# Kernel tuning notes

Measured on AMD Instinct MI355X. Metric: run time of the kernel, lower is better.

Reference implementation:

```python
import jax, jax.numpy as jnp
import numpy as np

NUM_HEADS = 16
ROT_DIM = 128  # == head_dim here
ROPE_BASE = 10000.0

def _deinterleave(t):
    # non-HF RoPE layout fix: cat(even channels, odd channels) along head_dim
    return jnp.concatenate([t[..., ::2], t[..., 1::2]], axis=-1)

def _rope(t, cos, sin):
    # t: [B,S,H,D]; rotary applied to first ROT_DIM dims with half-split (GPT-NeoX style)
    rot, rest = t[..., :ROT_DIM], t[..., ROT_DIM:]
    x1, x2 = rot[..., : ROT_DIM // 2], rot[..., ROT_DIM // 2 :]
    c = cos[None, :, None, :]
    s = sin[None, :, None, :]
    rot = jnp.concatenate([x1 * c - x2 * s, x1 * s + x2 * c], axis=-1)
    return jnp.concatenate([rot, rest], axis=-1) if rest.shape[-1] else rot

def setup_inputs() -> dict:
    key = jax.random.key(0)
    ks = jax.random.split(key, 5)
    B, S, E = 4, 2048, 2048
    return {
        "x": jax.random.normal(ks[0], (B, S, E), jnp.float32),
        "wqkv_w": jax.random.normal(ks[1], (3 * E, E), jnp.float32) * (E ** -0.5),
        "wqkv_b": jax.random.normal(ks[2], (3 * E,), jnp.float32) * 0.01,
        "wo_w": jax.random.normal(ks[3], (E, E), jnp.float32) * (E ** -0.5),
        "wo_b": jax.random.normal(ks[4], (E,), jnp.float32) * 0.01,
    }

def reference(x, wqkv_w, wqkv_b, wo_w, wo_b):
    B, S, E = x.shape
    H = NUM_HEADS
    D = E // H
    scale = 1.0 / jnp.sqrt(jnp.asarray(D, x.dtype))
    # fused QKV projection; channel layout is (h, three, d)
    qkv = x @ wqkv_w.T + wqkv_b               # [B,S,3E]
    qkv = qkv.reshape(B, S, H, 3, D)
    q, k, v = qkv[..., 0, :], qkv[..., 1, :], qkv[..., 2, :]  # [B,S,H,D]
    # non-HF rotary layout shuffle on q,k only
    q = _deinterleave(q)
    k = _deinterleave(k)
    # rotary embedding
    inv_freq = 1.0 / (ROPE_BASE ** (jnp.arange(0, ROT_DIM, 2, dtype=jnp.float32) / ROT_DIM))
    t = jnp.arange(S, dtype=jnp.float32)
    freqs = jnp.outer(t, inv_freq)            # [S, ROT_DIM/2]
    cos, sin = jnp.cos(freqs).astype(x.dtype), jnp.sin(freqs).astype(x.dtype)
    q = _rope(q, cos, sin)
    k = _rope(k, cos, sin)
    # causal self-attention (vanilla, fp32 softmax)
    scores = jnp.einsum("bshd,bthd->bhst", q, k) * scale   # [B,H,S,S]
    causal = jnp.tril(jnp.ones((S, S), bool))
    scores = jnp.where(causal[None, None], scores, jnp.asarray(-1e4, scores.dtype))
    attn = jax.nn.softmax(scores.astype(jnp.float32), axis=-1).astype(scores.dtype)
    ctx = jnp.einsum("bhst,bthd->bshd", attn, v)           # [B,S,H,D]
    # output projection
    out = ctx.reshape(B, S, E) @ wo_w.T + wo_b
    return out
```

## Files before the change

kernel.cpp:

```cpp
#include <hip/hip_runtime.h>


using frag_ab = __attribute__((ext_vector_type(8))) short;
using frag_cd = __attribute__((ext_vector_type(4))) float;

__device__ __forceinline__ float b2f(unsigned short u) {
  union { unsigned int i; float f; } v; v.i = ((unsigned int)u) << 16; return v.f;
}
__device__ __forceinline__ unsigned short f2b(float f) {
  union { float f; unsigned int i; } v; v.f = f;
  unsigned int r = v.i + 0x7FFFu + ((v.i >> 16) & 1u);
  return (unsigned short)(r >> 16);
}
__device__ __forceinline__ unsigned int pack2(float a, float b) {
  return (unsigned int)f2b(a) | ((unsigned int)f2b(b) << 16);
}
__device__ __forceinline__ void gload16(const unsigned short* g, unsigned short* l) {
  __builtin_amdgcn_global_load_lds(
      (const __attribute__((address_space(1))) unsigned int*)g,
      (__attribute__((address_space(3))) unsigned int*)l, 16, 0, 0);
}

__global__ __launch_bounds__(256)
void cvt_f32_bf16(const float* __restrict__ in, unsigned short* __restrict__ out) {
  long i = (long)(blockIdx.x * 256 + threadIdx.x) * 8;
  float4 a = *(const float4*)&in[i];
  float4 b = *(const float4*)&in[i + 4];
  uint4 p;
  p.x = pack2(a.x, a.y); p.y = pack2(a.z, a.w);
  p.z = pack2(b.x, b.y); p.w = pack2(b.z, b.w);
  *(uint4*)&out[i] = p;
}

__device__ __forceinline__ void stage_a_async(const unsigned short* A, unsigned short* As,
                                              int row0, int k0, int wave, int lane, int ldk) {
#pragma unroll
  for (int i = 0; i < 4; i++) {
    int rbase = wave * 32 + i * 8;
    int r = rbase + (lane >> 3);
    int srcc = (lane & 7) ^ (r & 7);
    gload16(&A[(long)(row0 + r) * ldk + k0 + srcc * 8], &As[rbase * 64]);
  }
}
__device__ __forceinline__ void stage_b_cvt(const float* Bw, unsigned short* Bs,
                                            int row0, int k0, int tid) {
#pragma unroll
  for (int i = 0; i < 4; i++) {
    int c = tid + i * 256;
    int r = c >> 3, ch = c & 7;
    const float* src = &Bw[(long)(row0 + r) * 2048 + k0 + ch * 8];
    float4 v0 = *(const float4*)src;
    float4 v1 = *(const float4*)(src + 4);
    uint4 p;
    p.x = pack2(v0.x, v0.y); p.y = pack2(v0.z, v0.w);
    p.z = pack2(v1.x, v1.y); p.w = pack2(v1.z, v1.w);
    *(uint4*)&Bs[r * 64 + ((ch ^ (r & 7)) * 8)] = p;
  }
}

__global__ __launch_bounds__(256)
void gemm_qkv(const unsigned short* __restrict__ A,
              const float* __restrict__ Bw,
              const unsigned short* __restrict__ Bbf,
              const float* __restrict__ bias,
              unsigned short* __restrict__ Qb,
              unsigned short* __restrict__ Kb,
              unsigned short* __restrict__ Vt) {
  __shared__ __align__(16) unsigned short As[128 * 64];
  __shared__ __align__(16) unsigned short Bs[128 * 64];
  const int tid  = threadIdx.x;
  const int wave = tid >> 6, lane = tid & 63;
  const int quad = lane >> 4, l16 = lane & 15;
  const int wm = (wave & 1) * 64, wn = (wave >> 1) * 64;
  const int row0A = blockIdx.x * 128;
  const int row0B = blockIdx.y * 128;

  frag_cd acc[4][4];
#pragma unroll
  for (int i = 0; i < 4; i++)
#pragma unroll
    for (int j = 0; j < 4; j++) acc[i][j] = (frag_cd){0.f, 0.f, 0.f, 0.f};

  for (int k0 = 0; k0 < 2048; k0 += 64) {
    stage_a_async(A, As, row0A, k0, wave, lane, 2048);
    if (Bbf) stage_a_async(Bbf, Bs, row0B, k0, wave, lane, 2048);
    else     stage_b_cvt(Bw, Bs, row0B, k0, tid);
    __syncthreads();
#pragma unroll
    for (int kk = 0; kk < 64; kk += 32) {
      frag_ab af[4], bf[4];
#pragma unroll
      for (int mi = 0; mi < 4; mi++) {
        int row = wm + mi * 16 + l16;
        af[mi] = *(const frag_ab*)&As[row * 64 + (((quad + (kk >> 3)) ^ (l16 & 7)) * 8)];
      }
#pragma unroll
      for (int ni = 0; ni < 4; ni++) {
        int row = wn + ni * 16 + l16;
        bf[ni] = *(const frag_ab*)&Bs[row * 64 + (((quad + (kk >> 3)) ^ (l16 & 7)) * 8)];
      }
#pragma unroll
      for (int mi = 0; mi < 4; mi++)
#pragma unroll
        for (int ni = 0; ni < 4; ni++)
          acc[mi][ni] = __builtin_amdgcn_mfma_f32_16x16x32_bf16(af[mi], bf[ni], acc[mi][ni], 0, 0, 0);
    }
    __syncthreads();
  }
#pragma unroll
  for (int ni = 0; ni < 4; ni++) {
    int col  = row0B + wn + ni * 16 + l16;
    int h    = col / 384;
    int rem  = col - h * 384;
    int slot = rem >> 7;
    int d    = rem & 127;
    float bv = bias[col];
#pragma unroll
    for (int mi = 0; mi < 4; mi++) {
#pragma unroll
      for (int r = 0; r < 4; r++) {
        int row = row0A + wm + mi * 16 + quad * 4 + r;
        int b = row >> 11, s = row & 2047;
        unsigned short val = f2b(acc[mi][ni][r] + bv);
        if (slot == 0)      Qb[((long)(b * 16 + h) * 2048 + s) * 128 + d] = val;
        else if (slot == 1) Kb[((long)(b * 16 + h) * 2048 + s) * 128 + d] = val;
        else                Vt[((long)(b * 16 + h) * 128 + d) * 2048 + s] = val;
      }
    }
  }
}

__global__ __launch_bounds__(256)
void rope_inplace(unsigned short* __restrict__ Qb, unsigned short* __restrict__ Kb) {
  int wid  = blockIdx.x * 4 + (threadIdx.x >> 6);
  int j    = threadIdx.x & 63;
  int part = wid & 1;
  int s    = (wid >> 1) & 2047;
  int bh   = wid >> 12;
  unsigned short* buf = part ? Kb : Qb;
  long base = ((long)bh * 2048 + s) * 128;
  unsigned int pr = *(const unsigned int*)&buf[base + 2 * j];
  float x1 = b2f((unsigned short)(pr & 0xFFFFu));
  float x2 = b2f((unsigned short)(pr >> 16));
  float inv = powf(10000.0f, -(float)(2 * j) / 128.0f);
  float ang = (float)s * inv;
  float sn, cs;
  sincosf(ang, &sn, &cs);
  buf[base + j]      = f2b(x1 * cs - x2 * sn);
  buf[base + 64 + j] = f2b(x1 * sn + x2 * cs);
}

__global__ __launch_bounds__(256)
void attn_fwd(const unsigned short* __restrict__ Q,
              const unsigned short* __restrict__ K,
              const unsigned short* __restrict__ Vt,
              unsigned short* __restrict__ ctx) {
  __shared__ __align__(16) unsigned short Ks[64 * 128];
  __shared__ __align__(16) unsigned short Vs[128 * 72];
  __shared__ __align__(16) unsigned short Ps[4][32 * 72];
  const int bh = blockIdx.x;
  const int qt = blockIdx.y;
  const int tid = threadIdx.x;
  const int wave = tid >> 6, lane = tid & 63;
  const int quad = lane >> 4, l16 = lane & 15;
  const long base = (long)bh * 2048 * 128;
  const int q0 = qt * 128 + wave * 32;
  const float scale = 0.08838834764831845f;

  frag_ab qf[2][4];
#pragma unroll
  for (int mi = 0; mi < 2; mi++)
#pragma unroll
    for (int ks = 0; ks < 4; ks++)
      qf[mi][ks] = *(const frag_ab*)&Q[base + (long)(q0 + mi * 16 + l16) * 128 + ks * 32 + quad * 8];

  frag_cd o[2][8];
#pragma unroll
  for (int mi = 0; mi < 2; mi++)
#pragma unroll
    for (int ni = 0; ni < 8; ni++) o[mi][ni] = (frag_cd){0.f, 0.f, 0.f, 0.f};
  float m_i[2][4], l_i[2][4];
#pragma unroll
  for (int mi = 0; mi < 2; mi++)
#pragma unroll
    for (int r = 0; r < 4; r++) { m_i[mi][r] = -1.0e30f; l_i[mi][r] = 0.f; }

  const int kv_end = qt * 128 + 128;
  for (int kv0 = 0; kv0 < kv_end; kv0 += 64) {
    __syncthreads();
#pragma unroll
    for (int i = 0; i < 4; i++) {
      int rbase = (wave * 4 + i) * 4;
      int r = rbase + (lane >> 4);
      int srcc = (lane & 15) ^ (r & 15);
      gload16(&K[base + (long)(kv0 + r) * 128 + srcc * 8], &Ks[rbase * 128]);
    }
#pragma unroll
    for (int i = 0; i < 4; i++) {
      int c = tid + i * 256;
      int d = c >> 3, ch = c & 7;
      *(uint4*)&Vs[d * 72 + ch * 8] =
          *(const uint4*)&Vt[(long)bh * 262144 + (long)d * 2048 + kv0 + ch * 8];
    }
    __syncthreads();

    float p[2][4][4];
#pragma unroll
    for (int nj = 0; nj < 4; nj++) {
      frag_ab kf[4];
#pragma unroll
      for (int ks = 0; ks < 4; ks++) {
        int row = nj * 16 + l16;
        kf[ks] = *(const frag_ab*)&Ks[row * 128 + (((ks * 4 + quad) ^ (row & 15)) * 8)];
      }
#pragma unroll
      for (int mi = 0; mi < 2; mi++) {
        frag_cd acc = (frag_cd){0.f, 0.f, 0.f, 0.f};
#pragma unroll
        for (int ks = 0; ks < 4; ks++)
          acc = __builtin_amdgcn_mfma_f32_16x16x32_bf16(qf[mi][ks], kf[ks], acc, 0, 0, 0);
        int colg = kv0 + nj * 16 + l16;
#pragma unroll
        for (int r = 0; r < 4; r++) {
          int rowg = q0 + mi * 16 + quad * 4 + r;
          float sc = acc[r] * scale;
          p[mi][nj][r] = (colg <= rowg) ? sc : -10000.0f;
        }
      }
    }

#pragma unroll
    for (int mi = 0; mi < 2; mi++) {
#pragma unroll
      for (int r = 0; r < 4; r++) {
        float mx = fmaxf(fmaxf(p[mi][0][r], p[mi][1][r]), fmaxf(p[mi][2][r], p[mi][3][r]));
#pragma unroll
        for (int off = 1; off < 16; off <<= 1)
          mx = fmaxf(mx, __shfl_xor(mx, off, 64));
        float mnew  = fmaxf(m_i[mi][r], mx);
        float alpha = __expf(m_i[mi][r] - mnew);
        float rs = 0.f;
#pragma unroll
        for (int nj = 0; nj < 4; nj++) {
          float e = __expf(p[mi][nj][r] - mnew);
          p[mi][nj][r] = e;
          rs += e;
        }
#pragma unroll
        for (int off = 1; off < 16; off <<= 1)
          rs += __shfl_xor(rs, off, 64);
        l_i[mi][r] = l_i[mi][r] * alpha + rs;
        m_i[mi][r] = mnew;
#pragma unroll
        for (int ni = 0; ni < 8; ni++) o[mi][ni][r] *= alpha;
      }
    }

    unsigned short* pw = &Ps[wave][0];
#pragma unroll
    for (int mi = 0; mi < 2; mi++)
#pragma unroll
      for (int nj = 0; nj < 4; nj++)
#pragma unroll
        for (int r = 0; r < 4; r++)
          pw[(mi * 16 + quad * 4 + r) * 72 + nj * 16 + l16] = f2b(p[mi][nj][r]);
    __syncthreads();

#pragma unroll
    for (int ni = 0; ni < 8; ni++) {
      frag_ab vf0 = *(const frag_ab*)&Vs[(ni * 16 + l16) * 72 + quad * 8];
      frag_ab vf1 = *(const frag_ab*)&Vs[(ni * 16 + l16) * 72 + 32 + quad * 8];
#pragma unroll
      for (int mi = 0; mi < 2; mi++) {
        frag_ab pf0 = *(const frag_ab*)&pw[(mi * 16 + l16) * 72 + quad * 8];
        frag_ab pf1 = *(const frag_ab*)&pw[(mi * 16 + l16) * 72 + 32 + quad * 8];
        o[mi][ni] = __builtin_amdgcn_mfma_f32_16x16x32_bf16(pf0, vf0, o[mi][ni], 0, 0, 0);
        o[mi][ni] = __builtin_amdgcn_mfma_f32_16x16x32_bf16(pf1, vf1, o[mi][ni], 0, 0, 0);
      }
    }
  }

  const int b = bh >> 4, h = bh & 15;
#pragma unroll
  for (int mi = 0; mi < 2; mi++) {
#pragma unroll
    for (int r = 0; r < 4; r++) {
      float inv = 1.0f / fmaxf(l_i[mi][r], 1.0e-20f);
      int s = q0 + mi * 16 + quad * 4 + r;
      long rowb = ((long)b * 2048 + s) * 2048 + h * 128;
#pragma unroll
      for (int ni = 0; ni < 8; ni++)
        ctx[rowb + ni * 16 + l16] = f2b(o[mi][ni][r] * inv);
    }
  }
}

__global__ __launch_bounds__(256)
void gemm_ctx(const unsigned short* __restrict__ A,
              const float* __restrict__ Bw,
              const unsigned short* __restrict__ Bbf,
              const float* __restrict__ bias,
              float* __restrict__ C) {
  __shared__ __align__(16) unsigned short As[128 * 64];
  __shared__ __align__(16) unsigned short Bs[128 * 64];
  const int tid  = threadIdx.x;
  const int wave = tid >> 6, lane = tid & 63;
  const int quad = lane >> 4, l16 = lane & 15;
  const int wm = (wave & 1) * 64, wn = (wave >> 1) * 64;
  const int row0A = blockIdx.x * 128;
  const int row0B = blockIdx.y * 128;

  frag_cd acc[4][4];
#pragma unroll
  for (int i = 0; i < 4; i++)
#pragma unroll
    for (int j = 0; j < 4; j++) acc[i][j] = (frag_cd){0.f, 0.f, 0.f, 0.f};

  for (int k0 = 0; k0 < 2048; k0 += 64) {
    stage_a_async(A, As, row0A, k0, wave, lane, 2048);
    if (Bbf) stage_a_async(Bbf, Bs, row0B, k0, wave, lane, 2048);
    else     stage_b_cvt(Bw, Bs, row0B, k0, tid);
    __syncthreads();
#pragma unroll
    for (int kk = 0; kk < 64; kk += 32) {
      frag_ab af[4], bf[4];
#pragma unroll
      for (int mi = 0; mi < 4; mi++) {
        int row = wm + mi * 16 + l16;
        af[mi] = *(const frag_ab*)&As[row * 64 + (((quad + (kk >> 3)) ^ (l16 & 7)) * 8)];
      }
#pragma unroll
      for (int ni = 0; ni < 4; ni++) {
        int row = wn + ni * 16 + l16;
        bf[ni] = *(const frag_ab*)&Bs[row * 64 + (((quad + (kk >> 3)) ^ (l16 & 7)) * 8)];
      }
#pragma unroll
      for (int mi = 0; mi < 4; mi++)
#pragma unroll
        for (int ni = 0; ni < 4; ni++)
          acc[mi][ni] = __builtin_amdgcn_mfma_f32_16x16x32_bf16(af[mi], bf[ni], acc[mi][ni], 0, 0, 0);
    }
    __syncthreads();
  }
#pragma unroll
  for (int ni = 0; ni < 4; ni++) {
    int col = row0B + wn + ni * 16 + l16;
    float bv = bias[col];
#pragma unroll
    for (int mi = 0; mi < 4; mi++) {
#pragma unroll
      for (int r = 0; r < 4; r++) {
        int row = row0A + wm + mi * 16 + quad * 4 + r;
        C[(long)row * 2048 + col] = acc[mi][ni][r] + bv;
      }
    }
  }
}

extern "C" void kernel_launch(void* const* d_in, const int* in_sizes, int n_in,
                              void* d_out, int out_size, void* d_ws, size_t ws_size,
                              hipStream_t stream) {
  const float* x      = (const float*)d_in[0];
  const float* wqkv_w = (const float*)d_in[1];
  const float* wqkv_b = (const float*)d_in[2];
  const float* wo_w   = (const float*)d_in[3];
  const float* wo_b   = (const float*)d_in[4];

  unsigned short* xb  = (unsigned short*)d_out;
  unsigned short* Qb  = (unsigned short*)d_out + 16777216;
  unsigned short* Kb  = (unsigned short*)d_ws;
  unsigned short* Vt  = (unsigned short*)d_ws + 16777216;
  unsigned short* ctx = (unsigned short*)d_out;
  float* outf = (float*)d_ws;

  const bool big = ws_size >= 100663296UL;
  unsigned short* Wq = big ? (unsigned short*)d_ws + 33554432 : nullptr;
  unsigned short* Wo = big ? (unsigned short*)d_ws + 46137344 : nullptr;

  cvt_f32_bf16<<<8192, 256, 0, stream>>>(x, xb);
  if (big) {
    cvt_f32_bf16<<<6144, 256, 0, stream>>>(wqkv_w, Wq);
    cvt_f32_bf16<<<2048, 256, 0, stream>>>(wo_w, Wo);
  }
  gemm_qkv<<<dim3(64, 48), 256, 0, stream>>>(xb, wqkv_w, Wq, wqkv_b, Qb, Kb, Vt);
  rope_inplace<<<65536, 256, 0, stream>>>(Qb, Kb);
  attn_fwd<<<dim3(64, 16), 256, 0, stream>>>(Qb, Kb, Vt, ctx);
  gemm_ctx<<<dim3(64, 16), 256, 0, stream>>>(ctx, wo_w, Wo, wo_b, outf);
  hipMemcpyAsync(d_out, outf, 67108864UL, hipMemcpyDeviceToDevice, stream);
}
```

Before: 831.5 us.

## Pair causal query tiles per block, async swizzled V loads, fold scale into RoPE

Each attention block now handles two query tiles (qt and 15-qt), so every block does the same amount of causal work, and the grid is halved. V tiles are loaded with global_load_lds into an XOR-swizzled unpadded LDS layout, replacing register-staged copies. Waves skip key tiles that lie fully above their causal rows, and the barrier before PV is removed. The MFMA phases are raised with s_setprio. The softmax scale is folded into Q during RoPE, which costs a slight bf16 rounding difference.

```diff
diff --git a/kernel.cpp b/kernel.cpp
--- a/kernel.cpp
+++ b/kernel.cpp
@@ -146,6 +146,8 @@
   float ang = (float)s * inv;
   float sn, cs;
   sincosf(ang, &sn, &cs);
+  float sc = part ? 1.0f : 0.08838834764831845f;
+  cs *= sc; sn *= sc;
   buf[base + j]      = f2b(x1 * cs - x2 * sn);
   buf[base + 64 + j] = f2b(x1 * sn + x2 * cs);
 }
@@ -156,76 +158,134 @@
               const unsigned short* __restrict__ Vt,
               unsigned short* __restrict__ ctx) {
   __shared__ __align__(16) unsigned short Ks[64 * 128];
-  __shared__ __align__(16) unsigned short Vs[128 * 72];
+  __shared__ __align__(16) unsigned short Vs[128 * 64];
   __shared__ __align__(16) unsigned short Ps[4][32 * 72];
   const int bh = blockIdx.x;
-  const int qt = blockIdx.y;
   const int tid = threadIdx.x;
   const int wave = tid >> 6, lane = tid & 63;
   const int quad = lane >> 4, l16 = lane & 15;
-  const long base = (long)bh * 2048 * 128;
-  const int q0 = qt * 128 + wave * 32;
-  const float scale = 0.08838834764831845f;
-
-  frag_ab qf[2][4];
-#pragma unroll
-  for (int mi = 0; mi < 2; mi++)
-#pragma unroll
-    for (int ks = 0; ks < 4; ks++)
-      qf[mi][ks] = *(const frag_ab*)&Q[base + (long)(q0 + mi * 16 + l16) * 128 + ks * 32 + quad * 8];
-
-  frag_cd o[2][8];
-#pragma unroll
-  for (int mi = 0; mi < 2; mi++)
-#pragma unroll
-    for (int ni = 0; ni < 8; ni++) o[mi][ni] = (frag_cd){0.f, 0.f, 0.f, 0.f};
-  float m_i[2][4], l_i[2][4];
-#pragma unroll
-  for (int mi = 0; mi < 2; mi++)
-#pragma unroll
-    for (int r = 0; r < 4; r++) { m_i[mi][r] = -1.0e30f; l_i[mi][r] = 0.f; }
-
-  const int kv_end = qt * 128 + 128;
-  for (int kv0 = 0; kv0 < kv_end; kv0 += 64) {
-    __syncthreads();
-#pragma unroll
-    for (int i = 0; i < 4; i++) {
-      int rbase = (wave * 4 + i) * 4;
-      int r = rbase + (lane >> 4);
-      int srcc = (lane & 15) ^ (r & 15);
-      gload16(&K[base + (long)(kv0 + r) * 128 + srcc * 8], &Ks[rbase * 128]);
-    }
-#pragma unroll
-    for (int i = 0; i < 4; i++) {
-      int c = tid + i * 256;
-      int d = c >> 3, ch = c & 7;
-      *(uint4*)&Vs[d * 72 + ch * 8] =
-          *(const uint4*)&Vt[(long)bh * 262144 + (long)d * 2048 + kv0 + ch * 8];
-    }
-    __syncthreads();
-
-    float p[2][4][4];
-#pragma unroll
-    for (int nj = 0; nj < 4; nj++) {
-      frag_ab kf[4];
-#pragma unroll
-      for (int ks = 0; ks < 4; ks++) {
-        int row = nj * 16 + l16;
-        kf[ks] = *(const frag_ab*)&Ks[row * 128 + (((ks * 4 + quad) ^ (row & 15)) * 8)];
-      }
-#pragma unroll
-      for (int mi = 0; mi < 2; mi++) {
-        frag_cd acc = (frag_cd){0.f, 0.f, 0.f, 0.f};
-#pragma unroll
-        for (int ks = 0; ks < 4; ks++)
-          acc = __builtin_amdgcn_mfma_f32_16x16x32_bf16(qf[mi][ks], kf[ks], acc, 0, 0, 0);
-        int colg = kv0 + nj * 16 + l16;
-#pragma unroll
-        for (int r = 0; r < 4; r++) {
-          int rowg = q0 + mi * 16 + quad * 4 + r;
-          float sc = acc[r] * scale;
-          p[mi][nj][r] = (colg <= rowg) ? sc : -10000.0f;
+  const long base  = (long)bh * 2048 * 128;
+  const long vbase = (long)bh * 262144;
+  const int b = bh >> 4, h = bh & 15;
+  unsigned short* pw = &Ps[wave][0];
+
+  for (int pass = 0; pass < 2; ++pass) {
+    const int qt = pass ? (15 - blockIdx.y) : blockIdx.y;
+    const int q0 = qt * 128 + wave * 32;
+
+    frag_ab qf[2][4];
+#pragma unroll
+    for (int mi = 0; mi < 2; mi++)
+#pragma unroll
+      for (int ks = 0; ks < 4; ks++)
+        qf[mi][ks] = *(const frag_ab*)&Q[base + (long)(q0 + mi * 16 + l16) * 128 + ks * 32 + quad * 8];
+
+    frag_cd o[2][8];
+#pragma unroll
+    for (int mi = 0; mi < 2; mi++)
+#pragma unroll
+      for (int ni = 0; ni < 8; ni++) o[mi][ni] = (frag_cd){0.f, 0.f, 0.f, 0.f};
+    float m_i[2][4], l_i[2][4];
+#pragma unroll
+    for (int mi = 0; mi < 2; mi++)
+#pragma unroll
+      for (int r = 0; r < 4; r++) { m_i[mi][r] = -1.0e30f; l_i[mi][r] = 0.f; }
+
+    const int kv_end = qt * 128 + 128;
+    for (int kv0 = 0; kv0 < kv_end; kv0 += 64) {
+      __syncthreads();
+#pragma unroll
+      for (int i = 0; i < 4; i++) {
+        int rbase = (wave * 4 + i) * 4;
+        int r = rbase + (lane >> 4);
+        int srcc = (lane & 15) ^ (r & 15);
+        gload16(&K[base + (long)(kv0 + r) * 128 + srcc * 8], &Ks[rbase * 128]);
+      }
+#pragma unroll
+      for (int i = 0; i < 4; i++) {
+        int rbase = wave * 32 + i * 8;
+        int r = rbase + (lane >> 3);
+        int srcc = (lane & 7) ^ (r & 7);
+        gload16(&Vt[vbase + (long)r * 2048 + kv0 + srcc * 8], &Vs[rbase * 64]);
+      }
+      __syncthreads();
+
+      if (kv0 <= q0 + 31) {
+        float p[2][4][4];
+        __builtin_amdgcn_s_setprio(1);
+#pragma unroll
+        for (int nj = 0; nj < 4; nj++) {
+          frag_ab kf[4];
+          int row = nj * 16 + l16;
+#pragma unroll
+          for (int ks = 0; ks < 4; ks++)
+            kf[ks] = *(const frag_ab*)&Ks[row * 128 + (((ks * 4 + quad) ^ (row & 15)) * 8)];
+#pragma unroll
+          for (int mi = 0; mi < 2; mi++) {
+            frag_cd acc = (frag_cd){0.f, 0.f, 0.f, 0.f};
+#pragma unroll
+            for (int ks = 0; ks < 4; ks++)
+              acc = __builtin_amdgcn_mfma_f32_16x16x32_bf16(qf[mi][ks], kf[ks], acc, 0, 0, 0);
+            int colg = kv0 + nj * 16 + l16;
+#pragma unroll
+            for (int r = 0; r < 4; r++) {
+              int rowg = q0 + mi * 16 + quad * 4 + r;
+              p[mi][nj][r] = (colg <= rowg) ? acc[r] : -10000.0f;
+            }
+          }
         }
+        __builtin_amdgcn_s_setprio(0);
+
+#pragma unroll
+        for (int mi = 0; mi < 2; mi++) {
+#pragma unroll
+          for (int r = 0; r < 4; r++) {
+            float mx = fmaxf(fmaxf(p[mi][0][r], p[mi][1][r]), fmaxf(p[mi][2][r], p[mi][3][r]));
+#pragma unroll
+            for (int off = 1; off < 16; off <<= 1)
+              mx = fmaxf(mx, __shfl_xor(mx, off, 64));
+            float mnew  = fmaxf(m_i[mi][r], mx);
+            float alpha = __expf(m_i[mi][r] - mnew);
+            float rs = 0.f;
+#pragma unroll
+            for (int nj = 0; nj < 4; nj++) {
+              float e = __expf(p[mi][nj][r] - mnew);
+              p[mi][nj][r] = e;
+              rs += e;
+            }
+#pragma unroll
+            for (int off = 1; off < 16; off <<= 1)
+              rs += __shfl_xor(rs, off, 64);
+            l_i[mi][r] = l_i[mi][r] * alpha + rs;
+            m_i[mi][r] = mnew;
+#pragma unroll
+            for (int ni = 0; ni < 8; ni++) o[mi][ni][r] *= alpha;
+          }
+        }
+
+#pragma unroll
+        for (int mi = 0; mi < 2; mi++)
+#pragma unroll
+          for (int nj = 0; nj < 4; nj++)
+#pragma unroll
+            for (int r = 0; r < 4; r++)
+              pw[(mi * 16 + quad * 4 + r) * 72 + nj * 16 + l16] = f2b(p[mi][nj][r]);
+
+        __builtin_amdgcn_s_setprio(1);
+#pragma unroll
+        for (int ni = 0; ni < 8; ni++) {
+          int vrow = ni * 16 + l16;
+          frag_ab vf0 = *(const frag_ab*)&Vs[vrow * 64 + ((quad ^ (l16 & 7)) * 8)];
+          frag_ab vf1 = *(const frag_ab*)&Vs[vrow * 64 + (((quad + 4) ^ (l16 & 7)) * 8)];
+#pragma unroll
+          for (int mi = 0; mi < 2; mi++) {
+            frag_ab pf0 = *(const frag_ab*)&pw[(mi * 16 + l16) * 72 + quad * 8];
+            frag_ab pf1 = *(const frag_ab*)&pw[(mi * 16 + l16) * 72 + 32 + quad * 8];
+            o[mi][ni] = __builtin_amdgcn_mfma_f32_16x16x32_bf16(pf0, vf0, o[mi][ni], 0, 0, 0);
+            o[mi][ni] = __builtin_amdgcn_mfma_f32_16x16x32_bf16(pf1, vf1, o[mi][ni], 0, 0, 0);
+          }
+        }
+        __builtin_amdgcn_s_setprio(0);
       }
     }
 
@@ -233,64 +293,13 @@
     for (int mi = 0; mi < 2; mi++) {
 #pragma unroll
       for (int r = 0; r < 4; r++) {
-        float mx = fmaxf(fmaxf(p[mi][0][r], p[mi][1][r]), fmaxf(p[mi][2][r], p[mi][3][r]));
-#pragma unroll
-        for (int off = 1; off < 16; off <<= 1)
-          mx = fmaxf(mx, __shfl_xor(mx, off, 64));
-        float mnew  = fmaxf(m_i[mi][r], mx);
-        float alpha = __expf(m_i[mi][r] - mnew);
-        float rs = 0.f;
-#pragma unroll
-        for (int nj = 0; nj < 4; nj++) {
-          float e = __expf(p[mi][nj][r] - mnew);
-          p[mi][nj][r] = e;
-          rs += e;
-        }
-#pragma unroll
-        for (int off = 1; off < 16; off <<= 1)
-          rs += __shfl_xor(rs, off, 64);
-        l_i[mi][r] = l_i[mi][r] * alpha + rs;
-        m_i[mi][r] = mnew;
-#pragma unroll
-        for (int ni = 0; ni < 8; ni++) o[mi][ni][r] *= alpha;
-      }
-    }
-
-    unsigned short* pw = &Ps[wave][0];
-#pragma unroll
-    for (int mi = 0; mi < 2; mi++)
-#pragma unroll
-      for (int nj = 0; nj < 4; nj++)
-#pragma unroll
-        for (int r = 0; r < 4; r++)
-          pw[(mi * 16 + quad * 4 + r) * 72 + nj * 16 + l16] = f2b(p[mi][nj][r]);
-    __syncthreads();
-
-#pragma unroll
-    for (int ni = 0; ni < 8; ni++) {
-      frag_ab vf0 = *(const frag_ab*)&Vs[(ni * 16 + l16) * 72 + quad * 8];
-      frag_ab vf1 = *(const frag_ab*)&Vs[(ni * 16 + l16) * 72 + 32 + quad * 8];
-#pragma unroll
-      for (int mi = 0; mi < 2; mi++) {
-        frag_ab pf0 = *(const frag_ab*)&pw[(mi * 16 + l16) * 72 + quad * 8];
-        frag_ab pf1 = *(const frag_ab*)&pw[(mi * 16 + l16) * 72 + 32 + quad * 8];
-        o[mi][ni] = __builtin_amdgcn_mfma_f32_16x16x32_bf16(pf0, vf0, o[mi][ni], 0, 0, 0);
-        o[mi][ni] = __builtin_amdgcn_mfma_f32_16x16x32_bf16(pf1, vf1, o[mi][ni], 0, 0, 0);
-      }
-    }
-  }
-
-  const int b = bh >> 4, h = bh & 15;
-#pragma unroll
-  for (int mi = 0; mi < 2; mi++) {
-#pragma unroll
-    for (int r = 0; r < 4; r++) {
-      float inv = 1.0f / fmaxf(l_i[mi][r], 1.0e-20f);
-      int s = q0 + mi * 16 + quad * 4 + r;
-      long rowb = ((long)b * 2048 + s) * 2048 + h * 128;
-#pragma unroll
-      for (int ni = 0; ni < 8; ni++)
-        ctx[rowb + ni * 16 + l16] = f2b(o[mi][ni][r] * inv);
+        float inv = 1.0f / fmaxf(l_i[mi][r], 1.0e-20f);
+        int s = q0 + mi * 16 + quad * 4 + r;
+        long rowb = ((long)b * 2048 + s) * 2048 + h * 128;
+#pragma unroll
+        for (int ni = 0; ni < 8; ni++)
+          ctx[rowb + ni * 16 + l16] = f2b(o[mi][ni][r] * inv);
+      }
     }
   }
 }
@@ -384,7 +393,7 @@
   }
   gemm_qkv<<<dim3(64, 48), 256, 0, stream>>>(xb, wqkv_w, Wq, wqkv_b, Qb, Kb, Vt);
   rope_inplace<<<65536, 256, 0, stream>>>(Qb, Kb);
-  attn_fwd<<<dim3(64, 16), 256, 0, stream>>>(Qb, Kb, Vt, ctx);
+  attn_fwd<<<dim3(64, 8), 256, 0, stream>>>(Qb, Kb, Vt, ctx);
   gemm_ctx<<<dim3(64, 16), 256, 0, stream>>>(ctx, wo_w, Wo, wo_b, outf);
   hipMemcpyAsync(d_out, outf, 67108864UL, hipMemcpyDeviceToDevice, stream);
 }
```

Result: faster. 798.8 us (-3.9%).
